# Performance work log

Measured on AMD Instinct MI355X. Metric: run time of the kernel, lower is better.

## Reference

```python
import jax, jax.numpy as jnp
import numpy as np

HEADS = 8
DIM_HEAD = 64


def setup_inputs() -> dict:
    key = jax.random.key(0)
    k1, k2, k3 = jax.random.split(key, 3)
    dim = 512
    hidden = HEADS * DIM_HEAD  # 512
    x = jax.random.normal(k1, (16, dim, 64, 64), dtype=jnp.float32)
    # 1x1 convs expressed as dense matrices (out_ch, in_ch)
    w_qkv = jax.random.normal(k2, (3 * hidden, dim), dtype=jnp.float32) * (1.0 / np.sqrt(dim))
    w_out = jax.random.normal(k3, (dim, hidden), dtype=jnp.float32) * (1.0 / np.sqrt(hidden))
    b_out = jnp.zeros((dim,), dtype=jnp.float32)
    return {"x": x, "w_qkv": w_qkv, "w_out": w_out, "b_out": b_out}


def reference(x, w_qkv, w_out, b_out):
    b, c, h, w = x.shape
    hw = h * w
    # 1x1 conv == channel matmul: (b, 3*hidden, hw)
    xf = x.reshape(b, c, hw)
    qkv = jnp.einsum('oc,bcn->bon', w_qkv, xf)
    # split into q,k,v each (b, heads, dim_head, hw)
    qkv = qkv.reshape(b, 3, HEADS, DIM_HEAD, hw)
    q, k, v = qkv[:, 0], qkv[:, 1], qkv[:, 2]
    k = jax.nn.softmax(k, axis=-1)  # softmax over spatial dim
    # context: (b, heads, dim_head, dim_head)
    context = jnp.einsum('bhcn,bhdn->bhcd', k, v)
    # out: context^T @ q -> (b, heads, dim_head, hw)
    out = jnp.einsum('bhcd,bhcn->bhdn', context, q)
    out = out.reshape(b, HEADS * DIM_HEAD, h, w)
    # to_out 1x1 conv with bias
    outf = out.reshape(b, HEADS * DIM_HEAD, hw)
    y = jnp.einsum('oc,bcn->bon', w_out, outf) + b_out[None, :, None]
    return y.reshape(b, -1, h, w)
```

## Files before the change

### kernel.cpp

```cpp
#include <hip/hip_runtime.h>
#include <string.h>

typedef __bf16 bf16x8 __attribute__((ext_vector_type(8)));
typedef float f32x4 __attribute__((ext_vector_type(4)));
typedef unsigned short u16;
typedef u16 u16x8 __attribute__((ext_vector_type(8)));

#define NB 16
#define CD 512
#define NN 4096
#define O3 1536

__device__ __forceinline__ u16 f2bf(float f) {
    union { float f; unsigned int u; } v; v.f = f;
    unsigned int r = v.u + 0x7fffu + ((v.u >> 16) & 1u);
    return (u16)(r >> 16);
}
__device__ __forceinline__ float bf2f(u16 s) {
    union { unsigned int u; float f; } v; v.u = ((unsigned int)s) << 16;
    return v.f;
}

__device__ __forceinline__ void gl2lds16(const u16* g, u16* l) {
    __builtin_amdgcn_global_load_lds(
        (const void __attribute__((address_space(1)))*)g,
        (void __attribute__((address_space(3)))*)l,
        16, 0, 0);
}

__global__ void k_convert(const float* __restrict__ in, u16* __restrict__ out, int n) {
    int i = blockIdx.x * 256 + threadIdx.x;
    if (i < n) out[i] = f2bf(in[i]);
}

__global__ __launch_bounds__(256) void k_transpose_x(const float* __restrict__ x,
                                                     u16* __restrict__ xt) {
    __shared__ float tile[64][65];
    const int b = blockIdx.y;
    const int ntile = blockIdx.x & 63;
    const int ctile = blockIdx.x >> 6;
    const int t = threadIdx.x;
    const int r = t >> 2;
    const int q = t & 3;

    const float* xb = x + ((size_t)b * CD + ctile * 64 + r) * NN + ntile * 64;
#pragma unroll
    for (int j = 0; j < 4; ++j) {
        float4 v = *(const float4*)&xb[q * 16 + j * 4];
        tile[r][q * 16 + j * 4 + 0] = v.x;
        tile[r][q * 16 + j * 4 + 1] = v.y;
        tile[r][q * 16 + j * 4 + 2] = v.z;
        tile[r][q * 16 + j * 4 + 3] = v.w;
    }
    __syncthreads();
    u16* xtb = xt + ((size_t)b * NN + ntile * 64 + r) * CD + ctile * 64 + q * 16;
    u16x8 o0, o1;
#pragma unroll
    for (int j = 0; j < 8; ++j) {
        o0[j] = f2bf(tile[q * 16 + j][r]);
        o1[j] = f2bf(tile[q * 16 + 8 + j][r]);
    }
    *(u16x8*)&xtb[0] = o0;
    *(u16x8*)&xtb[8] = o1;
}


__device__ __forceinline__ void lda8(const u16* p, bf16x8 (&aa)[4][2],
                                     int aoff, int sw0, int sw1) {
#pragma unroll
    for (int mi = 0; mi < 4; ++mi) {
        aa[mi][0] = *(const bf16x8*)&p[aoff + mi * 1024 + sw0];
        aa[mi][1] = *(const bf16x8*)&p[aoff + mi * 1024 + sw1];
    }
}

__device__ __forceinline__ void ldb4(const u16* p, bf16x8 (&bb)[2][2],
                                     int boff, int sw0, int sw1) {
#pragma unroll
    for (int ni = 0; ni < 2; ++ni) {
        bb[ni][0] = *(const bf16x8*)&p[boff + ni * 1024 + sw0];
        bb[ni][1] = *(const bf16x8*)&p[boff + ni * 1024 + sw1];
    }
}

__device__ __forceinline__ void mfma16(bf16x8 (&aa)[4][2], bf16x8 (&bb)[2][2],
                                       f32x4 (&ac)[4][2]) {
    __builtin_amdgcn_s_setprio(1);
#pragma unroll
    for (int mi = 0; mi < 4; ++mi)
#pragma unroll
        for (int ni = 0; ni < 2; ++ni) {
            ac[mi][ni] = __builtin_amdgcn_mfma_f32_16x16x32_bf16(
                aa[mi][0], bb[ni][0], ac[mi][ni], 0, 0, 0);
            ac[mi][ni] = __builtin_amdgcn_mfma_f32_16x16x32_bf16(
                aa[mi][1], bb[ni][1], ac[mi][ni], 0, 0, 0);
        }
    __builtin_amdgcn_s_setprio(0);
}

#define BAR() do { \
    asm volatile("" ::: "memory"); \
    __builtin_amdgcn_s_barrier(); \
    asm volatile("" ::: "memory"); \
} while (0)

__device__ __forceinline__ void gemm256_core(u16* __restrict__ smem,
                                             const u16* __restrict__ Abase,
                                             const u16* __restrict__ Bbase,
                                             f32x4 (&acc)[2][2][4][2]) {
    const int t = threadIdx.x;
    const int lane = t & 63;
    const int w = t >> 6;
    const int l15 = lane & 15, quad = lane >> 4;
    const int r0 = t >> 3;
    const int sg = ((t & 7) ^ (r0 & 7)) * 8;
    const int aoff = ((w >> 2) * 64 + l15) * 64;
    const int boff = ((w & 3) * 32 + l15) * 64;
    const int sw0 = ((0 + quad) ^ (l15 & 7)) * 8;
    const int sw1 = ((4 + quad) ^ (l15 & 7)) * 8;

    auto ldsAt = [&](int s, int op, int half) -> u16* {
        return smem + (size_t)(((s * 2 + op) * 2 + half) * 8192);
    };

    auto stage = [&](int op, int half, int tau) {
        const u16* s = (op ? Bbase : Abase)
                       + (size_t)(half * 128 + r0) * CD + tau * 64 + sg;
        u16* d = ldsAt(tau & 1, op, half) + t * 8;
        gl2lds16(s, d);
        gl2lds16(s + (size_t)64 * CD, d + 4096);
    };

    stage(0, 0, 0); stage(1, 0, 0); stage(1, 1, 0); stage(0, 1, 0);
    stage(0, 0, 1); stage(1, 0, 1);
    asm volatile("s_waitcnt vmcnt(4)" ::: "memory");
    BAR();

    bf16x8 aa[4][2], bb0[2][2], bb1[2][2];
    ldb4(ldsAt(0, 1, 0), bb0, boff, sw0, sw1);

    for (int kt = 0; kt < 8; ++kt) {
        const int s = kt & 1;
        lda8(ldsAt(s, 0, 0), aa, aoff, sw0, sw1);
        ldb4(ldsAt(s, 1, 1), bb1, boff, sw0, sw1);
        if (kt <= 6) { stage(1, 1, kt + 1); stage(0, 1, kt + 1); }
        mfma16(aa, bb0, acc[0][0]);
        BAR();
        if (kt <= 5) stage(0, 0, kt + 2);
        mfma16(aa, bb1, acc[0][1]);
        BAR();
        lda8(ldsAt(s, 0, 1), aa, aoff, sw0, sw1);
        if (kt <= 5) stage(1, 0, kt + 2);
        mfma16(aa, bb0, acc[1][0]);
        if (kt <= 5)      asm volatile("s_waitcnt vmcnt(4)" ::: "memory");
        else if (kt == 6) asm volatile("s_waitcnt vmcnt(0)" ::: "memory");
        BAR();
        if (kt <= 6) ldb4(ldsAt(s ^ 1, 1, 0), bb0, boff, sw0, sw1);
        mfma16(aa, bb1, acc[1][1]);
        BAR();
    }
}

__global__ __launch_bounds__(512, 2) void k_gemm1(
        const u16* __restrict__ A, const u16* __restrict__ Bt,
        u16* __restrict__ qt, u16* __restrict__ kbuf, u16* __restrict__ vbuf) {
    __shared__ __align__(16) u16 smem[65536];
    const int gid = blockIdx.x;
    const int u = (gid & 7) * 192 + (gid >> 3);
    const int mt = u % 6;
    const int bn = u / 6;
    const int b = bn >> 4;
    const int nt = bn & 15;
    const int t = threadIdx.x;
    const int lane = t & 63, w = t >> 6;
    const int l15 = lane & 15, quad = lane >> 4;

    f32x4 acc[2][2][4][2] = {};
    gemm256_core(smem, A + (size_t)(mt * 256) * CD,
                 Bt + ((size_t)b * NN + nt * 256) * CD, acc);

    const int sec = mt >> 1;
    const int lrb = mt * 256 - sec * 512;
#pragma unroll
    for (int qm = 0; qm < 2; ++qm)
#pragma unroll
    for (int mi = 0; mi < 4; ++mi) {
        const int ml = qm * 128 + (w >> 2) * 64 + mi * 16 + quad * 4;
#pragma unroll
        for (int qn = 0; qn < 2; ++qn)
#pragma unroll
        for (int ni = 0; ni < 2; ++ni) {
            const int n = nt * 256 + qn * 128 + (w & 3) * 32 + ni * 16 + l15;
            f32x4 v = acc[qm][qn][mi][ni];
            if (sec == 0) {
                ushort4 pk;
                pk.x = f2bf(v[0]); pk.y = f2bf(v[1]);
                pk.z = f2bf(v[2]); pk.w = f2bf(v[3]);
                *(ushort4*)&qt[((size_t)b * NN + n) * CD + mt * 256 + ml] = pk;
            } else {
                u16* dst = (sec == 1) ? kbuf : vbuf;
#pragma unroll
                for (int r = 0; r < 4; ++r)
                    dst[((size_t)(b * 512 + lrb + ml + r)) * NN + n] = f2bf(v[r]);
            }
        }
    }
}

__global__ __launch_bounds__(256) void k_ctx(const u16* __restrict__ kbuf,
                                             const u16* __restrict__ vbuf,
                                             float* __restrict__ ctxT,
                                             float* __restrict__ lsum) {
    const int bh = blockIdx.y;
    const int chunk = blockIdx.x;
    const int t = threadIdx.x, lane = t & 63, w = t >> 6;
    const int l15 = lane & 15, quad = lane >> 4;
    const int cb = w * 16;

    const u16* krow = kbuf + (size_t)(bh * 64 + cb + l15) * NN;
    const u16* vb   = vbuf + (size_t)bh * 64 * NN;

    f32x4 acc[4] = {};
    float ls = 0.f;
    for (int i = 0; i < 32; ++i) {
        int n0 = chunk * 1024 + i * 32 + quad * 8;
        u16x8 ku = *(const u16x8*)&krow[n0];
        u16x8 afu;
#pragma unroll
        for (int jj = 0; jj < 8; ++jj) {
            float ev = __expf(fminf(bf2f(ku[jj]), 30.f));
            ls += ev;
            afu[jj] = f2bf(ev);
        }
        bf16x8 af = __builtin_bit_cast(bf16x8, afu);
#pragma unroll
        for (int di = 0; di < 4; ++di) {
            bf16x8 bfv = *(const bf16x8*)&vb[(size_t)(di * 16 + l15) * NN + n0];
            acc[di] = __builtin_amdgcn_mfma_f32_16x16x32_bf16(af, bfv, acc[di], 0, 0, 0);
        }
    }
    ls += __shfl_xor(ls, 16);
    ls += __shfl_xor(ls, 32);
    if (quad == 0) atomicAdd(&lsum[(size_t)bh * 64 + cb + l15], ls);

    const int c = cb + quad * 4;
#pragma unroll
    for (int di = 0; di < 4; ++di) {
        int d = di * 16 + l15;
#pragma unroll
        for (int r = 0; r < 4; ++r)
            atomicAdd(&ctxT[((size_t)bh * 64 + d) * 64 + c + r], acc[di][r]);
    }
}

__global__ __launch_bounds__(256) void k_weff(const float* __restrict__ wout,
                                              const float* __restrict__ ctxT,
                                              const float* __restrict__ lsum,
                                              u16* __restrict__ weff) {
    int idx = blockIdx.x * 256 + threadIdx.x;
    int b = idx >> 18;
    int o = (idx >> 9) & 511;
    int hc = idx & 511;
    int h = hc >> 6, c = hc & 63;
    const float* wr = wout + o * 512 + h * 64;
    const float* cr = ctxT + ((size_t)b * 8 + h) * 4096 + c;
    float s = 0.f;
#pragma unroll
    for (int d = 0; d < 64; ++d) s += wr[d] * cr[d * 64];
    s *= 1.0f / lsum[((size_t)b * 8 + h) * 64 + c];
    weff[idx] = f2bf(s);
}

__global__ __launch_bounds__(512, 2) void k_gemm2(
        const u16* __restrict__ weff, const u16* __restrict__ qt,
        const float* __restrict__ bout, float* __restrict__ y) {
    __shared__ __align__(16) u16 smem[65536];
    const int gid = blockIdx.x;
    const int u = (gid & 7) * 64 + (gid >> 3);
    const int mt = u & 1;
    const int bn = u >> 1;
    const int b = bn >> 4;
    const int nt = bn & 15;
    const int t = threadIdx.x;
    const int lane = t & 63, w = t >> 6;
    const int l15 = lane & 15, quad = lane >> 4;

    f32x4 acc[2][2][4][2] = {};
    gemm256_core(smem, weff + (size_t)b * 512 * 512 + (size_t)(mt * 256) * CD,
                 qt + ((size_t)b * NN + nt * 256) * CD, acc);

#pragma unroll
    for (int qm = 0; qm < 2; ++qm)
#pragma unroll
    for (int mi = 0; mi < 4; ++mi) {
        const int o = mt * 256 + qm * 128 + (w >> 2) * 64 + mi * 16 + quad * 4;
#pragma unroll
        for (int qn = 0; qn < 2; ++qn)
#pragma unroll
        for (int ni = 0; ni < 2; ++ni) {
            const int n = nt * 256 + qn * 128 + (w & 3) * 32 + ni * 16 + l15;
            f32x4 v = acc[qm][qn][mi][ni];
#pragma unroll
            for (int r = 0; r < 4; ++r)
                y[((size_t)(b * 512 + o + r)) * NN + n] = v[r] + bout[o + r];
        }
    }
}

extern "C" void kernel_launch(void* const* d_in, const int* in_sizes, int n_in,
                              void* d_out, int out_size, void* d_ws, size_t ws_size,
                              hipStream_t stream) {
    const float* x    = (const float*)d_in[0];
    const float* wqkv = (const float*)d_in[1];
    const float* wout = (const float*)d_in[2];
    const float* bout = (const float*)d_in[3];
    float* y = (float*)d_out;

    char* ws = (char*)d_ws;
    u16*   xt   = (u16*)(ws);
    u16*   wqb  = (u16*)(ws + 67108864);
    u16*   qt   = (u16*)(ws + 68681728);
    u16*   kbuf = (u16*)(ws + 135790592);
    u16*   vbuf = (u16*)(ws + 202899456);
    float* ctxT = (float*)(ws + 270008320);
    float* lsum = (float*)(ws + 272105472);
    u16*   weff = (u16*)(ws + 272138240);

    hipMemsetAsync(ctxT, 0, 2097152 + 32768, stream);

    k_convert<<<(O3 * CD + 255) / 256, 256, 0, stream>>>(wqkv, wqb, O3 * CD);
    k_transpose_x<<<dim3(64 * 8, NB), 256, 0, stream>>>(x, xt);
    k_gemm1<<<1536, 512, 0, stream>>>(wqb, xt, qt, kbuf, vbuf);
    k_ctx<<<dim3(4, NB * 8), 256, 0, stream>>>(kbuf, vbuf, ctxT, lsum);
    k_weff<<<(NB * 512 * 512) / 256, 256, 0, stream>>>(wout, ctxT, lsum, weff);
    k_gemm2<<<512, 512, 0, stream>>>(weff, qt, bout, y);
}
```

Measured before the change: 517.3 us.

## Halve GEMM K-tile to BK=32 for 4 blocks/CU and split context reduction finer

The shared GEMM core now stages 32-wide K slices instead of 64, which halves LDS per block to 64 KB and raises launch bounds to allow 4 blocks per CU. The main loop becomes a simpler 16-step double-buffered loop with a new XOR swizzle and one barrier per step. The context kernel splits the spatial reduction into 8 chunks instead of 4 to expose more blocks. In exchange the GEMM has more barriers and full vmcnt(0) waits per K step, less prefetch depth, and register pressure under the tighter launch bound. The finer context split also doubles the atomic adds.

```diff
diff --git a/kernel.cpp b/kernel.cpp
--- a/kernel.cpp
+++ b/kernel.cpp
@@ -65,39 +65,6 @@
 }
 
 
-__device__ __forceinline__ void lda8(const u16* p, bf16x8 (&aa)[4][2],
-                                     int aoff, int sw0, int sw1) {
-#pragma unroll
-    for (int mi = 0; mi < 4; ++mi) {
-        aa[mi][0] = *(const bf16x8*)&p[aoff + mi * 1024 + sw0];
-        aa[mi][1] = *(const bf16x8*)&p[aoff + mi * 1024 + sw1];
-    }
-}
-
-__device__ __forceinline__ void ldb4(const u16* p, bf16x8 (&bb)[2][2],
-                                     int boff, int sw0, int sw1) {
-#pragma unroll
-    for (int ni = 0; ni < 2; ++ni) {
-        bb[ni][0] = *(const bf16x8*)&p[boff + ni * 1024 + sw0];
-        bb[ni][1] = *(const bf16x8*)&p[boff + ni * 1024 + sw1];
-    }
-}
-
-__device__ __forceinline__ void mfma16(bf16x8 (&aa)[4][2], bf16x8 (&bb)[2][2],
-                                       f32x4 (&ac)[4][2]) {
-    __builtin_amdgcn_s_setprio(1);
-#pragma unroll
-    for (int mi = 0; mi < 4; ++mi)
-#pragma unroll
-        for (int ni = 0; ni < 2; ++ni) {
-            ac[mi][ni] = __builtin_amdgcn_mfma_f32_16x16x32_bf16(
-                aa[mi][0], bb[ni][0], ac[mi][ni], 0, 0, 0);
-            ac[mi][ni] = __builtin_amdgcn_mfma_f32_16x16x32_bf16(
-                aa[mi][1], bb[ni][1], ac[mi][ni], 0, 0, 0);
-        }
-    __builtin_amdgcn_s_setprio(0);
-}
-
 #define BAR() do { \
     asm volatile("" ::: "memory"); \
     __builtin_amdgcn_s_barrier(); \
@@ -112,59 +79,78 @@
     const int lane = t & 63;
     const int w = t >> 6;
     const int l15 = lane & 15, quad = lane >> 4;
-    const int r0 = t >> 3;
-    const int sg = ((t & 7) ^ (r0 & 7)) * 8;
-    const int aoff = ((w >> 2) * 64 + l15) * 64;
-    const int boff = ((w & 3) * 32 + l15) * 64;
-    const int sw0 = ((0 + quad) ^ (l15 & 7)) * 8;
-    const int sw1 = ((4 + quad) ^ (l15 & 7)) * 8;
+    const int r0 = t >> 2;
+    const int sg = ((t & 3) ^ ((r0 >> 1) & 3)) * 8;
+    const int am = (w >> 2) * 64 + l15;
+    const int bn = (w & 3) * 32 + l15;
+    const int rsw = (quad ^ ((l15 >> 1) & 3)) << 3;
 
     auto ldsAt = [&](int s, int op, int half) -> u16* {
-        return smem + (size_t)(((s * 2 + op) * 2 + half) * 8192);
+        return smem + (size_t)(((s * 2 + op) * 2 + half) * 4096);
     };
-
     auto stage = [&](int op, int half, int tau) {
-        const u16* s = (op ? Bbase : Abase)
-                       + (size_t)(half * 128 + r0) * CD + tau * 64 + sg;
-        u16* d = ldsAt(tau & 1, op, half) + t * 8;
-        gl2lds16(s, d);
-        gl2lds16(s + (size_t)64 * CD, d + 4096);
+        const u16* src = (op ? Bbase : Abase)
+                         + (size_t)(half * 128 + r0) * CD + tau * 32 + sg;
+        gl2lds16(src, ldsAt(tau & 1, op, half) + t * 8);
     };
 
-    stage(0, 0, 0); stage(1, 0, 0); stage(1, 1, 0); stage(0, 1, 0);
-    stage(0, 0, 1); stage(1, 0, 1);
-    asm volatile("s_waitcnt vmcnt(4)" ::: "memory");
+    stage(0, 0, 0); stage(0, 1, 0); stage(1, 0, 0); stage(1, 1, 0);
+    asm volatile("s_waitcnt vmcnt(0)" ::: "memory");
     BAR();
 
-    bf16x8 aa[4][2], bb0[2][2], bb1[2][2];
-    ldb4(ldsAt(0, 1, 0), bb0, boff, sw0, sw1);
-
-    for (int kt = 0; kt < 8; ++kt) {
+    bf16x8 aa[4], bb0[2], bb1[2];
+    for (int kt = 0; kt < 16; ++kt) {
         const int s = kt & 1;
-        lda8(ldsAt(s, 0, 0), aa, aoff, sw0, sw1);
-        ldb4(ldsAt(s, 1, 1), bb1, boff, sw0, sw1);
-        if (kt <= 6) { stage(1, 1, kt + 1); stage(0, 1, kt + 1); }
-        mfma16(aa, bb0, acc[0][0]);
+        const u16* pa0 = ldsAt(s, 0, 0);
+        const u16* pa1 = ldsAt(s, 0, 1);
+        const u16* pb0 = ldsAt(s, 1, 0);
+        const u16* pb1 = ldsAt(s, 1, 1);
+#pragma unroll
+        for (int mi = 0; mi < 4; ++mi)
+            aa[mi] = *(const bf16x8*)&pa0[(am + mi * 16) * 32 + rsw];
+#pragma unroll
+        for (int ni = 0; ni < 2; ++ni) {
+            bb0[ni] = *(const bf16x8*)&pb0[(bn + ni * 16) * 32 + rsw];
+            bb1[ni] = *(const bf16x8*)&pb1[(bn + ni * 16) * 32 + rsw];
+        }
+        if (kt < 15) {
+            stage(0, 0, kt + 1); stage(0, 1, kt + 1);
+            stage(1, 0, kt + 1); stage(1, 1, kt + 1);
+        }
+        __builtin_amdgcn_s_setprio(1);
+#pragma unroll
+        for (int mi = 0; mi < 4; ++mi)
+#pragma unroll
+            for (int ni = 0; ni < 2; ++ni) {
+                acc[0][0][mi][ni] = __builtin_amdgcn_mfma_f32_16x16x32_bf16(
+                    aa[mi], bb0[ni], acc[0][0][mi][ni], 0, 0, 0);
+                acc[0][1][mi][ni] = __builtin_amdgcn_mfma_f32_16x16x32_bf16(
+                    aa[mi], bb1[ni], acc[0][1][mi][ni], 0, 0, 0);
+            }
+        __builtin_amdgcn_s_setprio(0);
+#pragma unroll
+        for (int mi = 0; mi < 4; ++mi)
+            aa[mi] = *(const bf16x8*)&pa1[(am + mi * 16) * 32 + rsw];
+        __builtin_amdgcn_s_setprio(1);
+#pragma unroll
+        for (int mi = 0; mi < 4; ++mi)
+#pragma unroll
+            for (int ni = 0; ni < 2; ++ni) {
+                acc[1][0][mi][ni] = __builtin_amdgcn_mfma_f32_16x16x32_bf16(
+                    aa[mi], bb0[ni], acc[1][0][mi][ni], 0, 0, 0);
+                acc[1][1][mi][ni] = __builtin_amdgcn_mfma_f32_16x16x32_bf16(
+                    aa[mi], bb1[ni], acc[1][1][mi][ni], 0, 0, 0);
+            }
+        __builtin_amdgcn_s_setprio(0);
+        if (kt < 15) asm volatile("s_waitcnt vmcnt(0)" ::: "memory");
         BAR();
-        if (kt <= 5) stage(0, 0, kt + 2);
-        mfma16(aa, bb1, acc[0][1]);
-        BAR();
-        lda8(ldsAt(s, 0, 1), aa, aoff, sw0, sw1);
-        if (kt <= 5) stage(1, 0, kt + 2);
-        mfma16(aa, bb0, acc[1][0]);
-        if (kt <= 5)      asm volatile("s_waitcnt vmcnt(4)" ::: "memory");
-        else if (kt == 6) asm volatile("s_waitcnt vmcnt(0)" ::: "memory");
-        BAR();
-        if (kt <= 6) ldb4(ldsAt(s ^ 1, 1, 0), bb0, boff, sw0, sw1);
-        mfma16(aa, bb1, acc[1][1]);
-        BAR();
-    }
-}
-
-__global__ __launch_bounds__(512, 2) void k_gemm1(
+    }
+}
+
+__global__ __launch_bounds__(512, 4) void k_gemm1(
         const u16* __restrict__ A, const u16* __restrict__ Bt,
         u16* __restrict__ qt, u16* __restrict__ kbuf, u16* __restrict__ vbuf) {
-    __shared__ __align__(16) u16 smem[65536];
+    __shared__ __align__(16) u16 smem[32768];
     const int gid = blockIdx.x;
     const int u = (gid & 7) * 192 + (gid >> 3);
     const int mt = u % 6;
@@ -222,8 +208,8 @@
 
     f32x4 acc[4] = {};
     float ls = 0.f;
-    for (int i = 0; i < 32; ++i) {
-        int n0 = chunk * 1024 + i * 32 + quad * 8;
+    for (int i = 0; i < 16; ++i) {
+        int n0 = chunk * 512 + i * 32 + quad * 8;
         u16x8 ku = *(const u16x8*)&krow[n0];
         u16x8 afu;
 #pragma unroll
@@ -271,10 +257,10 @@
     weff[idx] = f2bf(s);
 }
 
-__global__ __launch_bounds__(512, 2) void k_gemm2(
+__global__ __launch_bounds__(512, 4) void k_gemm2(
         const u16* __restrict__ weff, const u16* __restrict__ qt,
         const float* __restrict__ bout, float* __restrict__ y) {
-    __shared__ __align__(16) u16 smem[65536];
+    __shared__ __align__(16) u16 smem[32768];
     const int gid = blockIdx.x;
     const int u = (gid & 7) * 64 + (gid >> 3);
     const int mt = u & 1;
@@ -331,7 +317,7 @@
     k_convert<<<(O3 * CD + 255) / 256, 256, 0, stream>>>(wqkv, wqb, O3 * CD);
     k_transpose_x<<<dim3(64 * 8, NB), 256, 0, stream>>>(x, xt);
     k_gemm1<<<1536, 512, 0, stream>>>(wqb, xt, qt, kbuf, vbuf);
-    k_ctx<<<dim3(4, NB * 8), 256, 0, stream>>>(kbuf, vbuf, ctxT, lsum);
+    k_ctx<<<dim3(8, NB * 8), 256, 0, stream>>>(kbuf, vbuf, ctxT, lsum);
     k_weff<<<(NB * 512 * 512) / 256, 256, 0, stream>>>(wout, ctxT, lsum, weff);
     k_gemm2<<<512, 512, 0, stream>>>(weff, qt, bout, y);
 }
```

After: 1.400 ms. +170.6%, slower.
